# Kernel tuning notes

Hardware: AMD Instinct MI355X
Metric: run time of the kernel (lower is better)

## Reference

```python
import jax, jax.numpy as jnp
import numpy as np

KS = 3          # deform kernel size
N = KS * KS     # sampling points per output pixel
PAD = 1         # zero padding

def conv2d(x, w, stride, padding):
    return jax.lax.conv_general_dilated(
        x, w, (stride, stride), [(padding, padding), (padding, padding)],
        dimension_numbers=('NCHW', 'OIHW', 'NCHW'))

def _gather(x_flat, qx, qy, Wp):
    # x_flat: [b, c, Hp*Wp]; qx, qy: [b, h, w, N] int32 -> [b, c, h, w, N]
    b = qx.shape[0]; c = x_flat.shape[1]
    idx = (qx * Wp + qy).reshape(b, 1, -1)
    out = jnp.take_along_axis(x_flat, jnp.broadcast_to(idx, (b, c, idx.shape[-1])), axis=2)
    return out.reshape(b, c, qx.shape[1], qx.shape[2], qx.shape[3])

def deform_conv(x, w_off, b_off, w_conv):
    # learned per-pixel offsets: [b, 2N, h, w] (first N = x-offsets, last N = y-offsets)
    offset = conv2d(x, w_off, 1, PAD) + b_off[None, :, None, None]
    b, _, h, w = offset.shape
    x_pad = jnp.pad(x, ((0, 0), (0, 0), (PAD, PAD), (PAD, PAD)))
    Hp, Wp = x_pad.shape[2], x_pad.shape[3]
    # kernel-relative offsets p_n in {-1,0,1}^2
    pn_x, pn_y = jnp.meshgrid(jnp.arange(-(KS // 2), KS // 2 + 1),
                              jnp.arange(-(KS // 2), KS // 2 + 1), indexing='ij')
    p_n = jnp.concatenate([pn_x.reshape(-1), pn_y.reshape(-1)]).reshape(1, 2 * N, 1, 1)
    # base grid p_0 (1..h, 1..w in padded coordinates)
    p0_x, p0_y = jnp.meshgrid(jnp.arange(1, h + 1), jnp.arange(1, w + 1), indexing='ij')
    p_0 = jnp.concatenate([jnp.tile(p0_x[None], (N, 1, 1)),
                           jnp.tile(p0_y[None], (N, 1, 1))])[None]  # [1, 2N, h, w]
    p = (p_0 + p_n).astype(offset.dtype) + offset                   # [b, 2N, h, w]
    p = jnp.transpose(p, (0, 2, 3, 1))                              # [b, h, w, 2N]
    px, py = p[..., :N], p[..., N:]
    q = jnp.floor(jax.lax.stop_gradient(p))
    qlt_x = jnp.clip(q[..., :N], 0, Hp - 1); qlt_y = jnp.clip(q[..., N:], 0, Wp - 1)
    qrb_x = jnp.clip(q[..., :N] + 1, 0, Hp - 1); qrb_y = jnp.clip(q[..., N:] + 1, 0, Wp - 1)
    px = jnp.clip(px, 0, Hp - 1); py = jnp.clip(py, 0, Wp - 1)
    # bilinear weights (classic DCN formulation)
    g_lt = (1 + (qlt_x - px)) * (1 + (qlt_y - py))
    g_rb = (1 - (qrb_x - px)) * (1 - (qrb_y - py))
    g_lb = (1 + (qlt_x - px)) * (1 - (qrb_y - py))
    g_rt = (1 - (qrb_x - px)) * (1 + (qlt_y - py))
    x_flat = x_pad.reshape(b, x_pad.shape[1], -1)
    qi = lambda a: a.astype(jnp.int32)
    x_lt = _gather(x_flat, qi(qlt_x), qi(qlt_y), Wp)
    x_rb = _gather(x_flat, qi(qrb_x), qi(qrb_y), Wp)
    x_lb = _gather(x_flat, qi(qlt_x), qi(qrb_y), Wp)
    x_rt = _gather(x_flat, qi(qrb_x), qi(qlt_y), Wp)
    xo = (g_lt[:, None] * x_lt + g_rb[:, None] * x_rb
          + g_lb[:, None] * x_lb + g_rt[:, None] * x_rt)  # [b, c, h, w, N]
    c = xo.shape[1]
    # unfold N -> (ks, ks) blocks: [b, c, h*ks, w*ks]
    xo = xo.reshape(b, c, h, w, KS, KS).transpose(0, 1, 2, 4, 3, 5).reshape(b, c, h * KS, w * KS)
    return conv2d(xo, w_conv, KS, 0)  # stride=ks aggregation, no bias

def reference(x, w_off, b_off, w_conv, w_fc, b_fc):
    y = jax.nn.relu(deform_conv(x, w_off, b_off, w_conv))          # [b, 8, 28, 28]
    y = jax.lax.reduce_window(y, -jnp.inf, jax.lax.max,
                              (1, 1, 2, 2), (1, 1, 2, 2), 'VALID')  # [b, 8, 14, 14]
    y = y.reshape(y.shape[0], -1)
    return y @ w_fc.T + b_fc

def setup_inputs() -> dict:
    key = jax.random.key(0)
    k1, k2, k3, k4 = jax.random.split(key, 4)
    B = 4096
    return {
        'x': jax.random.normal(k1, (B, 1, 28, 28), dtype=jnp.float32),
        'w_off': jax.random.normal(k2, (18, 1, 3, 3), dtype=jnp.float32) * 0.1,
        'b_off': jnp.zeros((18,), dtype=jnp.float32),
        'w_conv': jax.random.normal(k3, (8, 1, 3, 3), dtype=jnp.float32) * 0.3,
        'w_fc': jax.random.normal(k4, (10, 8 * 14 * 14), dtype=jnp.float32) * 0.02,
        'b_fc': jnp.zeros((10,), dtype=jnp.float32),
    }
```

## Files before the change

### kernel.cpp

```cpp
#include <hip/hip_runtime.h>


#define HH 28
#define WW 28
#define WP 30
#define NPOS 784
#define NPOOL 1568
#define CELLS 196

__global__ __launch_bounds__(256) void deform_net_kernel(
    const float* __restrict__ x,
    const float* __restrict__ w_off,
    const float* __restrict__ b_off,
    const float* __restrict__ w_conv,
    const float* __restrict__ w_fc,
    const float* __restrict__ b_fc,
    float* __restrict__ out)
{
    __shared__ float xs[900];
    __shared__ float wo_s[162];
    __shared__ float bo_s[18];
    __shared__ float wc_s[72];
    __shared__ float red[4][10];

    const int b   = blockIdx.x;
    const int tid = threadIdx.x;

    if (tid < 162) wo_s[tid] = w_off[tid];
    if (tid < 18)  bo_s[tid] = b_off[tid];
    if (tid < 72)  wc_s[tid] = w_conv[tid];

    const float* xb = x + (size_t)b * NPOS;
    for (int i = tid; i < 900; i += 256) {
        int r = i / WP, c = i % WP;
        float v = 0.f;
        if (r >= 1 && r <= HH && c >= 1 && c <= WW)
            v = xb[(r - 1) * WW + (c - 1)];
        xs[i] = v;
    }
    __syncthreads();

    float fc[10];
    #pragma unroll
    for (int c = 0; c < 10; c++) fc[c] = 0.f;

    if (tid < CELLS) {
        const int ph = tid / 14, pw = tid % 14;
        const int h0 = 2 * ph, w0 = 2 * pw;

        float nb[16];
        #pragma unroll
        for (int i = 0; i < 4; i++)
            #pragma unroll
            for (int j = 0; j < 4; j++)
                nb[i * 4 + j] = xs[(h0 + i) * WP + (w0 + j)];

        float acc[4][8];
        #pragma unroll
        for (int p = 0; p < 4; p++)
            #pragma unroll
            for (int o = 0; o < 8; o++) acc[p][o] = 0.f;

        #pragma unroll
        for (int k = 0; k < 9; k++) {
            const int kx = k / 3, ky = k % 3;
            #pragma unroll
            for (int p = 0; p < 4; p++) {
                const int dh = p >> 1, dw = p & 1;

                float offx = bo_s[k], offy = bo_s[k + 9];
                #pragma unroll
                for (int t = 0; t < 9; t++) {
                    float nv = nb[(dh + t / 3) * 4 + (dw + t % 3)];
                    offx = fmaf(wo_s[k * 9 + t],       nv, offx);
                    offy = fmaf(wo_s[(k + 9) * 9 + t], nv, offy);
                }

                float p_x = (float)(h0 + dh + kx) + offx;
                float p_y = (float)(w0 + dw + ky) + offy;

                float q0x = floorf(p_x), q0y = floorf(p_y);
                float qltx = __builtin_amdgcn_fmed3f(q0x,       0.f, 29.f);
                float qlty = __builtin_amdgcn_fmed3f(q0y,       0.f, 29.f);
                float qrbx = __builtin_amdgcn_fmed3f(q0x + 1.f, 0.f, 29.f);
                float qrby = __builtin_amdgcn_fmed3f(q0y + 1.f, 0.f, 29.f);
                float px   = __builtin_amdgcn_fmed3f(p_x,       0.f, 29.f);
                float py   = __builtin_amdgcn_fmed3f(p_y,       0.f, 29.f);

                float gltx = 1.f + (qltx - px);
                float glty = 1.f + (qlty - py);
                float grbx = 1.f - (qrbx - px);
                float grby = 1.f - (qrby - py);

                int ilx = (int)qltx, ily = (int)qlty;
                int irx = (int)qrbx, iry = (int)qrby;

                float xlt = xs[ilx * WP + ily];
                float xrb = xs[irx * WP + iry];
                float xlb = xs[ilx * WP + iry];
                float xrt = xs[irx * WP + ily];

                float s = gltx * (glty * xlt + grby * xlb)
                        + grbx * (glty * xrt + grby * xrb);

                #pragma unroll
                for (int o = 0; o < 8; o++)
                    acc[p][o] = fmaf(wc_s[o * 9 + k], s, acc[p][o]);
            }
        }

        #pragma unroll
        for (int o = 0; o < 8; o++) {
            float m = fmaxf(fmaxf(acc[0][o], acc[1][o]),
                            fmaxf(acc[2][o], acc[3][o]));
            m = fmaxf(m, 0.f);
            const float* wrow = w_fc + o * CELLS + tid;
            #pragma unroll
            for (int c = 0; c < 10; c++)
                fc[c] = fmaf(m, wrow[c * NPOOL], fc[c]);
        }
    }

    #pragma unroll
    for (int c = 0; c < 10; c++) {
        #pragma unroll
        for (int sh = 32; sh > 0; sh >>= 1)
            fc[c] += __shfl_down(fc[c], sh, 64);
    }
    const int wave = tid >> 6, lane = tid & 63;
    if (lane == 0) {
        #pragma unroll
        for (int c = 0; c < 10; c++) red[wave][c] = fc[c];
    }
    __syncthreads();
    if (tid < 10)
        out[b * 10 + tid] = red[0][tid] + red[1][tid] + red[2][tid]
                          + red[3][tid] + b_fc[tid];
}

extern "C" void kernel_launch(void* const* d_in, const int* in_sizes, int n_in,
                              void* d_out, int out_size, void* d_ws, size_t ws_size,
                              hipStream_t stream) {
    const float* x      = (const float*)d_in[0];
    const float* w_off  = (const float*)d_in[1];
    const float* b_off  = (const float*)d_in[2];
    const float* w_conv = (const float*)d_in[3];
    const float* w_fc   = (const float*)d_in[4];
    const float* b_fc   = (const float*)d_in[5];
    float* out = (float*)d_out;

    const int B = in_sizes[0] / NPOS;
    deform_net_kernel<<<B, 256, 0, stream>>>(x, w_off, b_off, w_conv, w_fc, b_fc, out);
}
```

Baseline: 126.2 us.

## Shrink blocks to three waves and offload leftover cells to cleanup blocks

Blocks drop from 256 to 192 threads, so each image's main block covers 192 of its 196 pooled cells with three fully busy waves. The remaining 4 cells per image are computed by extra cleanup blocks that read directly from global memory, each handling 48 images. Partial FC results from both block types are combined with atomicAdd into an output zeroed by a memset. This removes the idle fourth wave but adds a memset, atomics and extra blocks with uncached global gathers.

```diff
diff --git a/kernel.cpp b/kernel.cpp
--- a/kernel.cpp
+++ b/kernel.cpp
@@ -1,52 +1,66 @@
 #include <hip/hip_runtime.h>
 
 
-#define HH 28
-#define WW 28
-#define WP 30
-#define NPOS 784
+#define NPOS  784
 #define NPOOL 1568
 #define CELLS 196
-
-__global__ __launch_bounds__(256) void deform_net_kernel(
+#define MAINC 192
+#define TPB   192
+#define WP    30
+#define PIMG  900
+#define CLIMG 48
+
+__device__ __forceinline__ float sample_unpadded(
+    const float* __restrict__ xb, int ix, int iy)
+{
+    unsigned ux = (unsigned)(ix - 1), uy = (unsigned)(iy - 1);
+    return (ux <= 27u && uy <= 27u) ? xb[ux * 28u + uy] : 0.f;
+}
+
+__global__ __launch_bounds__(192) void deform_net_kernel(
     const float* __restrict__ x,
     const float* __restrict__ w_off,
     const float* __restrict__ b_off,
     const float* __restrict__ w_conv,
     const float* __restrict__ w_fc,
     const float* __restrict__ b_fc,
-    float* __restrict__ out)
+    float* __restrict__ out,
+    int Btot)
 {
-    __shared__ float xs[900];
+    __shared__ float xs[PIMG];
     __shared__ float wo_s[162];
     __shared__ float bo_s[18];
     __shared__ float wc_s[72];
-    __shared__ float red[4][10];
-
-    const int b   = blockIdx.x;
+    __shared__ float red[3][10];
+
     const int tid = threadIdx.x;
+    const int bid = blockIdx.x;
+    const bool mainBlk = (bid < Btot);
 
     if (tid < 162) wo_s[tid] = w_off[tid];
     if (tid < 18)  bo_s[tid] = b_off[tid];
     if (tid < 72)  wc_s[tid] = w_conv[tid];
 
-    const float* xb = x + (size_t)b * NPOS;
-    for (int i = tid; i < 900; i += 256) {
-        int r = i / WP, c = i % WP;
-        float v = 0.f;
-        if (r >= 1 && r <= HH && c >= 1 && c <= WW)
-            v = xb[(r - 1) * WW + (c - 1)];
-        xs[i] = v;
+    if (mainBlk) {
+        const float* __restrict__ xb = x + (size_t)bid * NPOS;
+        for (int i = tid; i < PIMG; i += TPB) {
+            int r = i / WP, c = i - r * WP;
+            float v = 0.f;
+            if (r >= 1 && r <= 28 && c >= 1 && c <= 28)
+                v = xb[(r - 1) * 28 + (c - 1)];
+            xs[i] = v;
+        }
     }
     __syncthreads();
 
-    float fc[10];
-    #pragma unroll
-    for (int c = 0; c < 10; c++) fc[c] = 0.f;
-
-    if (tid < CELLS) {
-        const int ph = tid / 14, pw = tid % 14;
+    if (mainBlk) {
+        const int cell = tid;
+        const int ph = cell / 14, pw = cell - (cell / 14) * 14;
         const int h0 = 2 * ph, w0 = 2 * pw;
+
+        float fc[10];
+        #pragma unroll
+        for (int c = 0; c < 10; c++) fc[c] = 0.f;
 
         float nb[16];
         #pragma unroll
@@ -114,28 +128,125 @@
             float m = fmaxf(fmaxf(acc[0][o], acc[1][o]),
                             fmaxf(acc[2][o], acc[3][o]));
             m = fmaxf(m, 0.f);
-            const float* wrow = w_fc + o * CELLS + tid;
+            const float* wrow = w_fc + o * CELLS + cell;
             #pragma unroll
             for (int c = 0; c < 10; c++)
                 fc[c] = fmaf(m, wrow[c * NPOOL], fc[c]);
         }
+
+        #pragma unroll
+        for (int c = 0; c < 10; c++) {
+            #pragma unroll
+            for (int sh = 32; sh > 0; sh >>= 1)
+                fc[c] += __shfl_down(fc[c], sh, 64);
+        }
+        const int wave = tid >> 6, lane = tid & 63;
+        if (lane == 0) {
+            #pragma unroll
+            for (int c = 0; c < 10; c++) red[wave][c] = fc[c];
+        }
+        __syncthreads();
+        if (tid < 10)
+            atomicAdd(out + bid * 10 + tid,
+                      red[0][tid] + red[1][tid] + red[2][tid] + b_fc[tid]);
+    } else {
+        const int cb   = bid - Btot;
+        const int img  = cb * CLIMG + (tid >> 2);
+        const int cell = MAINC + (tid & 3);
+
+        float fc[10];
+        #pragma unroll
+        for (int c = 0; c < 10; c++) fc[c] = 0.f;
+
+        if (img < Btot) {
+            const float* __restrict__ xb = x + (size_t)img * NPOS;
+            const int ph = cell / 14, pw = cell - (cell / 14) * 14;
+            const int h0 = 2 * ph, w0 = 2 * pw;
+
+            float nb[16];
+            #pragma unroll
+            for (int i = 0; i < 4; i++)
+                #pragma unroll
+                for (int j = 0; j < 4; j++)
+                    nb[i * 4 + j] = sample_unpadded(xb, h0 + i, w0 + j);
+
+            float acc[4][8];
+            #pragma unroll
+            for (int p = 0; p < 4; p++)
+                #pragma unroll
+                for (int o = 0; o < 8; o++) acc[p][o] = 0.f;
+
+            #pragma unroll
+            for (int k = 0; k < 9; k++) {
+                const int kx = k / 3, ky = k % 3;
+                #pragma unroll
+                for (int p = 0; p < 4; p++) {
+                    const int dh = p >> 1, dw = p & 1;
+
+                    float offx = bo_s[k], offy = bo_s[k + 9];
+                    #pragma unroll
+                    for (int t = 0; t < 9; t++) {
+                        float nv = nb[(dh + t / 3) * 4 + (dw + t % 3)];
+                        offx = fmaf(wo_s[k * 9 + t],       nv, offx);
+                        offy = fmaf(wo_s[(k + 9) * 9 + t], nv, offy);
+                    }
+
+                    float p_x = (float)(h0 + dh + kx) + offx;
+                    float p_y = (float)(w0 + dw + ky) + offy;
+
+                    float q0x = floorf(p_x), q0y = floorf(p_y);
+                    float qltx = __builtin_amdgcn_fmed3f(q0x,       0.f, 29.f);
+                    float qlty = __builtin_amdgcn_fmed3f(q0y,       0.f, 29.f);
+                    float qrbx = __builtin_amdgcn_fmed3f(q0x + 1.f, 0.f, 29.f);
+                    float qrby = __builtin_amdgcn_fmed3f(q0y + 1.f, 0.f, 29.f);
+                    float px   = __builtin_amdgcn_fmed3f(p_x,       0.f, 29.f);
+                    float py   = __builtin_amdgcn_fmed3f(p_y,       0.f, 29.f);
+
+                    float gltx = 1.f + (qltx - px);
+                    float glty = 1.f + (qlty - py);
+                    float grbx = 1.f - (qrbx - px);
+                    float grby = 1.f - (qrby - py);
+
+                    int ilx = (int)qltx, ily = (int)qlty;
+                    int irx = (int)qrbx, iry = (int)qrby;
+
+                    float xlt = sample_unpadded(xb, ilx, ily);
+                    float xrb = sample_unpadded(xb, irx, iry);
+                    float xlb = sample_unpadded(xb, ilx, iry);
+                    float xrt = sample_unpadded(xb, irx, ily);
+
+                    float s = gltx * (glty * xlt + grby * xlb)
+                            + grbx * (glty * xrt + grby * xrb);
+
+                    #pragma unroll
+                    for (int o = 0; o < 8; o++)
+                        acc[p][o] = fmaf(wc_s[o * 9 + k], s, acc[p][o]);
+                }
+            }
+
+            #pragma unroll
+            for (int o = 0; o < 8; o++) {
+                float m = fmaxf(fmaxf(acc[0][o], acc[1][o]),
+                                fmaxf(acc[2][o], acc[3][o]));
+                m = fmaxf(m, 0.f);
+                const float* wrow = w_fc + o * CELLS + cell;
+                #pragma unroll
+                for (int c = 0; c < 10; c++)
+                    fc[c] = fmaf(m, wrow[c * NPOOL], fc[c]);
+            }
+        }
+
+        #pragma unroll
+        for (int c = 0; c < 10; c++) {
+            fc[c] += __shfl_xor(fc[c], 1, 64);
+            fc[c] += __shfl_xor(fc[c], 2, 64);
+        }
+        if ((tid & 3) == 0 && img < Btot) {
+            #pragma unroll
+            for (int c = 0; c < 10; c++)
+                atomicAdd(out + img * 10 + c, fc[c]);
+        }
     }
-
-    #pragma unroll
-    for (int c = 0; c < 10; c++) {
-        #pragma unroll
-        for (int sh = 32; sh > 0; sh >>= 1)
-            fc[c] += __shfl_down(fc[c], sh, 64);
-    }
-    const int wave = tid >> 6, lane = tid & 63;
-    if (lane == 0) {
-        #pragma unroll
-        for (int c = 0; c < 10; c++) red[wave][c] = fc[c];
-    }
-    __syncthreads();
-    if (tid < 10)
-        out[b * 10 + tid] = red[0][tid] + red[1][tid] + red[2][tid]
-                          + red[3][tid] + b_fc[tid];
 }
 
 extern "C" void kernel_launch(void* const* d_in, const int* in_sizes, int n_in,
@@ -150,5 +261,8 @@
     float* out = (float*)d_out;
 
     const int B = in_sizes[0] / NPOS;
-    deform_net_kernel<<<B, 256, 0, stream>>>(x, w_off, b_off, w_conv, w_fc, b_fc, out);
+    hipMemsetAsync(d_out, 0, (size_t)B * 10 * sizeof(float), stream);
+    const int nclean = (B + CLIMG - 1) / CLIMG;
+    deform_net_kernel<<<B + nclean, TPB, 0, stream>>>(
+        x, w_off, b_off, w_conv, w_fc, b_fc, out, B);
 }
```

Result: slower. 212.3 us (+68.2%).
